# Performance work log

Measured on AMD Instinct MI355X. Metric: run time of the kernel, lower is better.

The kernel has to match this reference:

```python
import jax, jax.numpy as jnp
import numpy as np

B, L, D, V = 512, 128, 512, 100000

def setup_inputs() -> dict:
    key = jax.random.key(0)
    ks = jax.random.split(key, 8)
    return {
        "t1s": jax.random.randint(ks[0], (B,), 0, V),
        "t2s": jax.random.randint(ks[1], (B,), 0, V),
        "t1_contexts": jax.random.randint(ks[2], (B, L), 0, V),
        "t2_contexts": jax.random.randint(ks[3], (B, L), 0, V),
        "embed_table": jax.random.normal(ks[4], (V, D), dtype=jnp.float32),
        "att_mat": jax.random.normal(ks[5], (D, D), dtype=jnp.float32) * (6.0 / (D + D)) ** 0.5,
        "w_pred": jax.random.normal(ks[6], (D, 1), dtype=jnp.float32) * 0.02,
        "b_pred": jnp.zeros((1,), dtype=jnp.float32),
    }

def _frob_normalize(x):
    # torch.norm(mat, p=2) is the Frobenius norm of the whole (L, D) matrix
    n = jnp.sqrt(jnp.sum(x * x, axis=(1, 2), keepdims=True))
    return x / n

def reference(t1s, t2s, t1_contexts, t2_contexts, embed_table, att_mat, w_pred, b_pred):
    # dropout is identity in eval mode; t1s/t2s embeddings are unused in the
    # 'dynamic' branch (dead code in the original forward).
    A = _frob_normalize(embed_table[t1_contexts])  # (B, L, D)
    Bm = _frob_normalize(embed_table[t2_contexts])  # (B, L, D)
    # batched bilinear attention: tanh(A @ att_mat @ B^T)
    S = jnp.tanh(jnp.einsum('bld,de,bme->blm', A, att_mat, Bm))  # (B, L, L)
    rows = jax.nn.softmax(jnp.mean(S, axis=2), axis=1)  # (B, L)
    cols = jax.nn.softmax(jnp.mean(S, axis=1), axis=1)  # (B, L)
    newA = jnp.einsum('bld,bl->bd', A, rows)   # (B, D)
    newB = jnp.einsum('bld,bl->bd', Bm, cols)  # (B, D)
    logits = ((newA * newB) @ w_pred + b_pred).reshape(-1)  # (B,)
    return logits, S
```

## Files before the change

kernel.cpp:

```cpp
#include <hip/hip_runtime.h>
#include <hip/hip_bf16.h>
#include <stdint.h>

#define NB 512
#define NL 128
#define ND 512

typedef __bf16 bf16;
typedef __bf16 bf16x8 __attribute__((ext_vector_type(8)));
typedef float  f32x4  __attribute__((ext_vector_type(4)));

#define GLDS(src, dst) __builtin_amdgcn_global_load_lds( \
    (const __attribute__((address_space(1))) void*)(src), \
    (__attribute__((address_space(3))) void*)(dst), 16, 0, 0)

__global__ __launch_bounds__(256) void k_attT(const float* __restrict__ att,
                                              bf16* __restrict__ attT) {
    int i = blockIdx.x * 256 + threadIdx.x;
    int n = i >> 9, k = i & 511;
    attT[i] = (bf16)att[k * 512 + n];
}

__global__ __launch_bounds__(512) void k_mega(
        const int* __restrict__ ctx1, const int* __restrict__ ctx2,
        const float* __restrict__ table, const bf16* __restrict__ attT,
        bf16* __restrict__ Ab, bf16* __restrict__ Bb,
        float* __restrict__ Sout, const float* __restrict__ w_pred,
        const float* __restrict__ b_pred, float* __restrict__ logits) {
    const int b = blockIdx.x, row0 = b * NL, tid = threadIdx.x;
    const int lane = tid & 63, w = tid >> 6;
    const int lm = lane & 15, quad = lane >> 4;

    __shared__ __align__(16) char smem[163840];
    bf16* sA0 = (bf16*)smem;
    bf16* sA1 = (bf16*)(smem + 8192);
    bf16* sT0 = (bf16*)(smem + 16384);
    bf16* sT1 = (bf16*)(smem + 49152);
    bf16* Tls = (bf16*)smem;
    bf16* sB0 = (bf16*)(smem + 131072);
    bf16* sB1 = (bf16*)(smem + 139264);
    bf16* sC0 = (bf16*)(smem + 147456);
    bf16* sC1 = (bf16*)(smem + 155648);
    float* red  = (float*)(smem + 1024);
    float* rowb = (float*)smem;
    float* colb = (float*)(smem + 2048);
    float* wrow = (float*)(smem + 3072);
    float* wcol = (float*)(smem + 3584);
    float* red2 = (float*)(smem + 2048);

    const int r8 = tid >> 6, c8 = tid & 63;
    float pa = 0.f, pb = 0.f;
    #pragma unroll 4
    for (int j = 0; j < 16; ++j) {
        int l = j * 8 + r8;
        int ia = ctx1[row0 + l], ib = ctx2[row0 + l];
        const float4* ra = (const float4*)table + (size_t)ia * (ND / 4) + c8 * 2;
        const float4* rb = (const float4*)table + (size_t)ib * (ND / 4) + c8 * 2;
        float4 a0 = ra[0], a1 = ra[1];
        float4 b0 = rb[0], b1 = rb[1];
        pa += a0.x*a0.x + a0.y*a0.y + a0.z*a0.z + a0.w*a0.w
            + a1.x*a1.x + a1.y*a1.y + a1.z*a1.z + a1.w*a1.w;
        pb += b0.x*b0.x + b0.y*b0.y + b0.z*b0.z + b0.w*b0.w
            + b1.x*b1.x + b1.y*b1.y + b1.z*b1.z + b1.w*b1.w;
        union { bf16 h[8]; uint4 u; } ua, ub;
        ua.h[0]=(bf16)a0.x; ua.h[1]=(bf16)a0.y; ua.h[2]=(bf16)a0.z; ua.h[3]=(bf16)a0.w;
        ua.h[4]=(bf16)a1.x; ua.h[5]=(bf16)a1.y; ua.h[6]=(bf16)a1.z; ua.h[7]=(bf16)a1.w;
        ub.h[0]=(bf16)b0.x; ub.h[1]=(bf16)b0.y; ub.h[2]=(bf16)b0.z; ub.h[3]=(bf16)b0.w;
        ub.h[4]=(bf16)b1.x; ub.h[5]=(bf16)b1.y; ub.h[6]=(bf16)b1.z; ub.h[7]=(bf16)b1.w;
        *(uint4*)(Ab + (size_t)(row0 + l) * ND + c8 * 8) = ua.u;
        *(uint4*)(Bb + (size_t)(row0 + l) * ND + c8 * 8) = ub.u;
    }
    for (int o = 32; o; o >>= 1) { pa += __shfl_xor(pa, o); pb += __shfl_xor(pb, o); }
    if (lane == 0) { red[w * 2] = pa; red[w * 2 + 1] = pb; }
    __syncthreads();
    float ssA = 0.f, ssB = 0.f;
    #pragma unroll
    for (int i = 0; i < 8; ++i) { ssA += red[i * 2]; ssB += red[i * 2 + 1]; }
    __syncthreads();

    const int wm1 = (w & 1) * 64;
    const int wn1 = (w >> 1) * 128;
    f32x4 acc1[4][8] = {};
    const int rA = tid >> 2, cA = tid & 3;

    GLDS(Ab + (size_t)(row0 + rA) * ND + cA * 8, sA0 + tid * 8);
    #pragma unroll
    for (int i = 0; i < 4; ++i) {
        int s = i * 512 + tid, r = s >> 2, c = s & 3;
        GLDS(attT + (size_t)r * ND + c * 8, sT0 + s * 8);
    }
    __syncthreads();

    for (int t = 0; t < 16; ++t) {
        if (t < 15) {
            const int k0 = (t + 1) * 32;
            bf16* dA = (t & 1) ? sA0 : sA1;
            bf16* dT = (t & 1) ? sT0 : sT1;
            GLDS(Ab + (size_t)(row0 + rA) * ND + k0 + cA * 8, dA + tid * 8);
            #pragma unroll
            for (int i = 0; i < 4; ++i) {
                int s = i * 512 + tid, r = s >> 2, c = s & 3;
                GLDS(attT + (size_t)r * ND + k0 + c * 8, dT + s * 8);
            }
        } else {
            GLDS(Bb + (size_t)(row0 + rA) * ND + cA * 8, sB0 + tid * 8);
            GLDS(Ab + (size_t)(row0 + rA) * ND + cA * 8, sC0 + tid * 8);
        }
        const bf16* A_ = (t & 1) ? sA1 : sA0;
        const bf16* T_ = (t & 1) ? sT1 : sT0;
        bf16x8 af[4], bfm[8];
        #pragma unroll
        for (int t4 = 0; t4 < 4; ++t4)
            af[t4] = *(const bf16x8*)&A_[(wm1 + t4 * 16 + lm) * 32 + quad * 8];
        #pragma unroll
        for (int t8 = 0; t8 < 8; ++t8)
            bfm[t8] = *(const bf16x8*)&T_[(wn1 + t8 * 16 + lm) * 32 + quad * 8];
        #pragma unroll
        for (int im = 0; im < 4; ++im)
            #pragma unroll
            for (int jn = 0; jn < 8; ++jn)
                acc1[im][jn] = __builtin_amdgcn_mfma_f32_16x16x32_bf16(
                    af[im], bfm[jn], acc1[im][jn], 0, 0, 0);
        __syncthreads();
    }

    #pragma unroll
    for (int im = 0; im < 4; ++im)
    #pragma unroll
    for (int jn = 0; jn < 8; ++jn)
    #pragma unroll
    for (int p = 0; p < 4; ++p) {
        int m = wm1 + im * 16 + quad * 4 + p;
        int n = wn1 + jn * 16 + lm;
        int ks = n >> 5, kq = (n >> 3) & 3, e = n & 7;
        int pos = kq ^ ((m >> 2) & 3);
        Tls[ks * 4096 + m * 32 + pos * 8 + e] = (bf16)acc1[im][jn][p];
    }
    __syncthreads();

    const int wm2 = (w & 1) * 64;
    const int wn2 = (w >> 1) * 32;
    f32x4 acc2[4][2] = {}, accG[4][2] = {};

    for (int t = 0; t < 16; ++t) {
        if (t < 15) {
            bf16* dB = (t & 1) ? sB0 : sB1;
            bf16* dC = (t & 1) ? sC0 : sC1;
            GLDS(Bb + (size_t)(row0 + rA) * ND + (t + 1) * 32 + cA * 8, dB + tid * 8);
            GLDS(Ab + (size_t)(row0 + rA) * ND + (t + 1) * 32 + cA * 8, dC + tid * 8);
        }
        const bf16* B_ = (t & 1) ? sB1 : sB0;
        const bf16* C_ = (t & 1) ? sC1 : sC0;
        float4 w0 = *(const float4*)(w_pred + t * 32 + quad * 8);
        float4 w1 = *(const float4*)(w_pred + t * 32 + quad * 8 + 4);
        float wv[8] = {w0.x, w0.y, w0.z, w0.w, w1.x, w1.y, w1.z, w1.w};
        bf16x8 af[4], af2[4], bf2[2], bfw[2];
        #pragma unroll
        for (int t4 = 0; t4 < 4; ++t4) {
            int r = wm2 + t4 * 16 + lm;
            af[t4]  = *(const bf16x8*)&Tls[t * 4096 + r * 32 + ((quad ^ ((r >> 2) & 3))) * 8];
            af2[t4] = *(const bf16x8*)&C_[r * 32 + quad * 8];
        }
        #pragma unroll
        for (int t2 = 0; t2 < 2; ++t2) {
            bf2[t2] = *(const bf16x8*)&B_[(wn2 + t2 * 16 + lm) * 32 + quad * 8];
            #pragma unroll
            for (int j = 0; j < 8; ++j)
                bfw[t2][j] = (bf16)((float)bf2[t2][j] * wv[j]);
        }
        #pragma unroll
        for (int im = 0; im < 4; ++im)
            #pragma unroll
            for (int jn = 0; jn < 2; ++jn) {
                acc2[im][jn] = __builtin_amdgcn_mfma_f32_16x16x32_bf16(
                    af[im], bf2[jn], acc2[im][jn], 0, 0, 0);
                accG[im][jn] = __builtin_amdgcn_mfma_f32_16x16x32_bf16(
                    af2[im], bfw[jn], accG[im][jn], 0, 0, 0);
            }
        __syncthreads();
    }

    const float sc = rsqrtf(ssA * ssB);
    float* __restrict__ Sb = Sout + (size_t)b * NL * NL;
    #pragma unroll
    for (int im = 0; im < 4; ++im)
    #pragma unroll
    for (int jn = 0; jn < 2; ++jn)
    #pragma unroll
    for (int p = 0; p < 4; ++p) {
        float v = tanhf(acc2[im][jn][p] * sc);
        acc2[im][jn][p] = v;
        int m = wm2 + im * 16 + quad * 4 + p;
        int n = wn2 + jn * 16 + lm;
        __builtin_nontemporal_store(v, &Sb[m * NL + n]);
    }
    #pragma unroll
    for (int im = 0; im < 4; ++im)
    #pragma unroll
    for (int p = 0; p < 4; ++p) {
        float r = acc2[im][0][p] + acc2[im][1][p];
        r += __shfl_xor(r, 1); r += __shfl_xor(r, 2);
        r += __shfl_xor(r, 4); r += __shfl_xor(r, 8);
        if (lm == 0) rowb[(w >> 1) * NL + wm2 + im * 16 + quad * 4 + p] = r;
    }
    #pragma unroll
    for (int jn = 0; jn < 2; ++jn) {
        float cv = 0.f;
        #pragma unroll
        for (int im = 0; im < 4; ++im)
            #pragma unroll
            for (int p = 0; p < 4; ++p) cv += acc2[im][jn][p];
        cv += __shfl_xor(cv, 16); cv += __shfl_xor(cv, 32);
        if (quad == 0) colb[(w & 1) * NL + wn2 + jn * 16 + lm] = cv;
    }
    __syncthreads();

    if (tid < 64) {
        float a  = (rowb[tid] + rowb[NL + tid] + rowb[2 * NL + tid] + rowb[3 * NL + tid]) * (1.f / NL);
        float c2 = (rowb[tid + 64] + rowb[NL + tid + 64] + rowb[2 * NL + tid + 64] + rowb[3 * NL + tid + 64]) * (1.f / NL);
        float mx = fmaxf(a, c2);
        for (int o = 32; o; o >>= 1) mx = fmaxf(mx, __shfl_xor(mx, o));
        float e0 = expf(a - mx), e1 = expf(c2 - mx);
        float s = e0 + e1;
        for (int o = 32; o; o >>= 1) s += __shfl_xor(s, o);
        float inv = 1.f / s;
        wrow[tid] = e0 * inv; wrow[tid + 64] = e1 * inv;
    } else if (tid < 128) {
        int q = tid - 64;
        float a  = (colb[q] + colb[NL + q]) * (1.f / NL);
        float c2 = (colb[q + 64] + colb[NL + q + 64]) * (1.f / NL);
        float mx = fmaxf(a, c2);
        for (int o = 32; o; o >>= 1) mx = fmaxf(mx, __shfl_xor(mx, o));
        float e0 = expf(a - mx), e1 = expf(c2 - mx);
        float s = e0 + e1;
        for (int o = 32; o; o >>= 1) s += __shfl_xor(s, o);
        float inv = 1.f / s;
        wcol[q] = e0 * inv; wcol[q + 64] = e1 * inv;
    }
    __syncthreads();

    float wc0 = wcol[wn2 + lm], wc1 = wcol[wn2 + 16 + lm];
    float g = 0.f;
    #pragma unroll
    for (int im = 0; im < 4; ++im)
    #pragma unroll
    for (int p = 0; p < 4; ++p) {
        float wr = wrow[wm2 + im * 16 + quad * 4 + p];
        g += wr * (wc0 * accG[im][0][p] + wc1 * accG[im][1][p]);
    }
    for (int o = 32; o; o >>= 1) g += __shfl_xor(g, o);
    if (lane == 0) red2[w] = g;
    __syncthreads();
    if (tid == 0) {
        float tot = 0.f;
        #pragma unroll
        for (int i = 0; i < 8; ++i) tot += red2[i];
        logits[b] = tot * sc + b_pred[0];
    }
}

extern "C" void kernel_launch(void* const* d_in, const int* in_sizes, int n_in,
                              void* d_out, int out_size, void* d_ws, size_t ws_size,
                              hipStream_t stream) {
    const int*   t1c = (const int*)d_in[2];
    const int*   t2c = (const int*)d_in[3];
    const float* emb = (const float*)d_in[4];
    const float* att = (const float*)d_in[5];
    const float* wp  = (const float*)d_in[6];
    const float* bp  = (const float*)d_in[7];

    float* out    = (float*)d_out;
    float* logits = out;
    float* S      = out + NB;

    char* ws = (char*)d_ws;
    bf16*  Ab   = (bf16*)(ws);
    bf16*  Bb   = (bf16*)(ws + 67108864);
    bf16*  attT = (bf16*)(ws + 134217728);

    k_attT<<<dim3(1024), 256, 0, stream>>>(att, attT);
    k_mega<<<dim3(NB), 512, 0, stream>>>(t1c, t2c, emb, attT, Ab, Bb,
                                         S, wp, bp, logits);
}
```

Measured before the change: 387.8 us.

## Chunk the attention GEMM over N to cut shared memory and raise occupancy

The first GEMM (A @ att) is now computed in four 128-column chunks, and each chunk is immediately consumed by the second GEMM against B, so the full T matrix no longer has to sit in shared memory. This shrinks LDS from 160KB to about 68KB, uses XOR-swizzled 64-wide K tiles, and adds a launch-bounds occupancy hint. The logits path is rebuilt as explicit weighted sums of A and B rows read back from global memory, replacing the extra MFMA accumulation. The trade-offs are no double buffering (load then sync each step), more barriers, and an extra global reread of A and B.

```diff
diff --git a/kernel.cpp b/kernel.cpp
--- a/kernel.cpp
+++ b/kernel.cpp
@@ -21,7 +21,7 @@
     attT[i] = (bf16)att[k * 512 + n];
 }
 
-__global__ __launch_bounds__(512) void k_mega(
+__global__ __launch_bounds__(512, 4) void k_mega(
         const int* __restrict__ ctx1, const int* __restrict__ ctx2,
         const float* __restrict__ table, const bf16* __restrict__ attT,
         bf16* __restrict__ Ab, bf16* __restrict__ Bb,
@@ -30,23 +30,21 @@
     const int b = blockIdx.x, row0 = b * NL, tid = threadIdx.x;
     const int lane = tid & 63, w = tid >> 6;
     const int lm = lane & 15, quad = lane >> 4;
-
-    __shared__ __align__(16) char smem[163840];
-    bf16* sA0 = (bf16*)smem;
-    bf16* sA1 = (bf16*)(smem + 8192);
-    bf16* sT0 = (bf16*)(smem + 16384);
-    bf16* sT1 = (bf16*)(smem + 49152);
-    bf16* Tls = (bf16*)smem;
-    bf16* sB0 = (bf16*)(smem + 131072);
-    bf16* sB1 = (bf16*)(smem + 139264);
-    bf16* sC0 = (bf16*)(smem + 147456);
-    bf16* sC1 = (bf16*)(smem + 155648);
-    float* red  = (float*)(smem + 1024);
-    float* rowb = (float*)smem;
-    float* colb = (float*)(smem + 2048);
-    float* wrow = (float*)(smem + 3072);
-    float* wcol = (float*)(smem + 3584);
-    float* red2 = (float*)(smem + 2048);
+    const int wm = (w & 1) * 64;
+    const int wn = (w >> 1) * 32;
+
+    __shared__ __align__(16) char smem[69888];
+    bf16* st0 = (bf16*)smem;
+    bf16* st1 = (bf16*)(smem + 16384);
+    bf16* Tch = (bf16*)(smem + 32768);
+    float* pA   = (float*)smem;
+    float* pB   = (float*)(smem + 16384);
+    float* red  = (float*)(smem + 65536);
+    float* red2 = (float*)(smem + 65600);
+    float* rowb = (float*)(smem + 65664);
+    float* colb = (float*)(smem + 67712);
+    float* wrow = (float*)(smem + 68736);
+    float* wcol = (float*)(smem + 69248);
 
     const int r8 = tid >> 6, c8 = tid & 63;
     float pa = 0.f, pb = 0.f;
@@ -76,107 +74,84 @@
     float ssA = 0.f, ssB = 0.f;
     #pragma unroll
     for (int i = 0; i < 8; ++i) { ssA += red[i * 2]; ssB += red[i * 2 + 1]; }
-    __syncthreads();
-
-    const int wm1 = (w & 1) * 64;
-    const int wn1 = (w >> 1) * 128;
-    f32x4 acc1[4][8] = {};
-    const int rA = tid >> 2, cA = tid & 3;
-
-    GLDS(Ab + (size_t)(row0 + rA) * ND + cA * 8, sA0 + tid * 8);
-    #pragma unroll
-    for (int i = 0; i < 4; ++i) {
-        int s = i * 512 + tid, r = s >> 2, c = s & 3;
-        GLDS(attT + (size_t)r * ND + c * 8, sT0 + s * 8);
-    }
-    __syncthreads();
-
-    for (int t = 0; t < 16; ++t) {
-        if (t < 15) {
-            const int k0 = (t + 1) * 32;
-            bf16* dA = (t & 1) ? sA0 : sA1;
-            bf16* dT = (t & 1) ? sT0 : sT1;
-            GLDS(Ab + (size_t)(row0 + rA) * ND + k0 + cA * 8, dA + tid * 8);
-            #pragma unroll
-            for (int i = 0; i < 4; ++i) {
-                int s = i * 512 + tid, r = s >> 2, c = s & 3;
-                GLDS(attT + (size_t)r * ND + k0 + c * 8, dT + s * 8);
-            }
-        } else {
-            GLDS(Bb + (size_t)(row0 + rA) * ND + cA * 8, sB0 + tid * 8);
-            GLDS(Ab + (size_t)(row0 + rA) * ND + cA * 8, sC0 + tid * 8);
-        }
-        const bf16* A_ = (t & 1) ? sA1 : sA0;
-        const bf16* T_ = (t & 1) ? sT1 : sT0;
-        bf16x8 af[4], bfm[8];
-        #pragma unroll
-        for (int t4 = 0; t4 < 4; ++t4)
-            af[t4] = *(const bf16x8*)&A_[(wm1 + t4 * 16 + lm) * 32 + quad * 8];
-        #pragma unroll
-        for (int t8 = 0; t8 < 8; ++t8)
-            bfm[t8] = *(const bf16x8*)&T_[(wn1 + t8 * 16 + lm) * 32 + quad * 8];
+
+    f32x4 accS[4][2] = {};
+
+    for (int nc = 0; nc < 4; ++nc) {
+        const bf16* attN = attT + (size_t)(nc * 128) * ND;
+        f32x4 acc1[4][2] = {};
+
+        for (int t8 = 0; t8 < 8; ++t8) {
+            const int k0 = t8 * 64;
+            #pragma unroll
+            for (int i = 0; i < 2; ++i) {
+                int s = i * 512 + tid, r = s >> 3, c = (s & 7) ^ (r & 7);
+                GLDS(Ab + (size_t)(row0 + r) * ND + k0 + c * 8, st0 + s * 8);
+                GLDS(attN + (size_t)r * ND + k0 + c * 8, st1 + s * 8);
+            }
+            __syncthreads();
+            #pragma unroll
+            for (int kk = 0; kk < 2; ++kk) {
+                bf16x8 af[4], bf2[2];
+                const int ca = (kk * 4 + quad) ^ (lm & 7);
+                #pragma unroll
+                for (int t4 = 0; t4 < 4; ++t4)
+                    af[t4] = *(const bf16x8*)&st0[(wm + t4 * 16 + lm) * 64 + ca * 8];
+                #pragma unroll
+                for (int t2 = 0; t2 < 2; ++t2)
+                    bf2[t2] = *(const bf16x8*)&st1[(wn + t2 * 16 + lm) * 64 + ca * 8];
+                #pragma unroll
+                for (int im = 0; im < 4; ++im)
+                    #pragma unroll
+                    for (int jn = 0; jn < 2; ++jn)
+                        acc1[im][jn] = __builtin_amdgcn_mfma_f32_16x16x32_bf16(
+                            af[im], bf2[jn], acc1[im][jn], 0, 0, 0);
+            }
+            __syncthreads();
+        }
+
+        #pragma unroll
+        for (int i = 0; i < 2; ++i) {
+            int s = i * 512 + tid, r = s >> 3, c = (s & 7) ^ (r & 7);
+            GLDS(Bb + (size_t)(row0 + r) * ND + nc * 128 + c * 8, st0 + s * 8);
+            GLDS(Bb + (size_t)(row0 + r) * ND + nc * 128 + 64 + c * 8, st1 + s * 8);
+        }
         #pragma unroll
         for (int im = 0; im < 4; ++im)
-            #pragma unroll
-            for (int jn = 0; jn < 8; ++jn)
-                acc1[im][jn] = __builtin_amdgcn_mfma_f32_16x16x32_bf16(
-                    af[im], bfm[jn], acc1[im][jn], 0, 0, 0);
+        #pragma unroll
+        for (int jn = 0; jn < 2; ++jn)
+        #pragma unroll
+        for (int p = 0; p < 4; ++p) {
+            int m = wm + im * 16 + quad * 4 + p;
+            int n = wn + jn * 16 + lm;
+            int ks = n >> 6, c = n & 63;
+            int pos = (((c >> 3) ^ (m & 7)) << 3) + (c & 7);
+            Tch[ks * 8192 + m * 64 + pos] = (bf16)acc1[im][jn][p];
+        }
         __syncthreads();
-    }
-
-    #pragma unroll
-    for (int im = 0; im < 4; ++im)
-    #pragma unroll
-    for (int jn = 0; jn < 8; ++jn)
-    #pragma unroll
-    for (int p = 0; p < 4; ++p) {
-        int m = wm1 + im * 16 + quad * 4 + p;
-        int n = wn1 + jn * 16 + lm;
-        int ks = n >> 5, kq = (n >> 3) & 3, e = n & 7;
-        int pos = kq ^ ((m >> 2) & 3);
-        Tls[ks * 4096 + m * 32 + pos * 8 + e] = (bf16)acc1[im][jn][p];
-    }
-    __syncthreads();
-
-    const int wm2 = (w & 1) * 64;
-    const int wn2 = (w >> 1) * 32;
-    f32x4 acc2[4][2] = {}, accG[4][2] = {};
-
-    for (int t = 0; t < 16; ++t) {
-        if (t < 15) {
-            bf16* dB = (t & 1) ? sB0 : sB1;
-            bf16* dC = (t & 1) ? sC0 : sC1;
-            GLDS(Bb + (size_t)(row0 + rA) * ND + (t + 1) * 32 + cA * 8, dB + tid * 8);
-            GLDS(Ab + (size_t)(row0 + rA) * ND + (t + 1) * 32 + cA * 8, dC + tid * 8);
-        }
-        const bf16* B_ = (t & 1) ? sB1 : sB0;
-        const bf16* C_ = (t & 1) ? sC1 : sC0;
-        float4 w0 = *(const float4*)(w_pred + t * 32 + quad * 8);
-        float4 w1 = *(const float4*)(w_pred + t * 32 + quad * 8 + 4);
-        float wv[8] = {w0.x, w0.y, w0.z, w0.w, w1.x, w1.y, w1.z, w1.w};
-        bf16x8 af[4], af2[4], bf2[2], bfw[2];
-        #pragma unroll
-        for (int t4 = 0; t4 < 4; ++t4) {
-            int r = wm2 + t4 * 16 + lm;
-            af[t4]  = *(const bf16x8*)&Tls[t * 4096 + r * 32 + ((quad ^ ((r >> 2) & 3))) * 8];
-            af2[t4] = *(const bf16x8*)&C_[r * 32 + quad * 8];
-        }
-        #pragma unroll
-        for (int t2 = 0; t2 < 2; ++t2) {
-            bf2[t2] = *(const bf16x8*)&B_[(wn2 + t2 * 16 + lm) * 32 + quad * 8];
-            #pragma unroll
-            for (int j = 0; j < 8; ++j)
-                bfw[t2][j] = (bf16)((float)bf2[t2][j] * wv[j]);
-        }
-        #pragma unroll
-        for (int im = 0; im < 4; ++im)
-            #pragma unroll
-            for (int jn = 0; jn < 2; ++jn) {
-                acc2[im][jn] = __builtin_amdgcn_mfma_f32_16x16x32_bf16(
-                    af[im], bf2[jn], acc2[im][jn], 0, 0, 0);
-                accG[im][jn] = __builtin_amdgcn_mfma_f32_16x16x32_bf16(
-                    af2[im], bfw[jn], accG[im][jn], 0, 0, 0);
-            }
+
+        #pragma unroll
+        for (int th = 0; th < 2; ++th) {
+            const bf16* Bs_ = th ? st1 : st0;
+            const bf16* Tk  = Tch + th * 8192;
+            #pragma unroll
+            for (int kk = 0; kk < 2; ++kk) {
+                bf16x8 af[4], bf2[2];
+                const int ca = (kk * 4 + quad) ^ (lm & 7);
+                #pragma unroll
+                for (int t4 = 0; t4 < 4; ++t4)
+                    af[t4] = *(const bf16x8*)&Tk[(wm + t4 * 16 + lm) * 64 + ca * 8];
+                #pragma unroll
+                for (int t2 = 0; t2 < 2; ++t2)
+                    bf2[t2] = *(const bf16x8*)&Bs_[(wn + t2 * 16 + lm) * 64 + ca * 8];
+                #pragma unroll
+                for (int im = 0; im < 4; ++im)
+                    #pragma unroll
+                    for (int jn = 0; jn < 2; ++jn)
+                        accS[im][jn] = __builtin_amdgcn_mfma_f32_16x16x32_bf16(
+                            af[im], bf2[jn], accS[im][jn], 0, 0, 0);
+            }
+        }
         __syncthreads();
     }
 
@@ -188,20 +163,20 @@
     for (int jn = 0; jn < 2; ++jn)
     #pragma unroll
     for (int p = 0; p < 4; ++p) {
-        float v = tanhf(acc2[im][jn][p] * sc);
-        acc2[im][jn][p] = v;
-        int m = wm2 + im * 16 + quad * 4 + p;
-        int n = wn2 + jn * 16 + lm;
+        float v = tanhf(accS[im][jn][p] * sc);
+        accS[im][jn][p] = v;
+        int m = wm + im * 16 + quad * 4 + p;
+        int n = wn + jn * 16 + lm;
         __builtin_nontemporal_store(v, &Sb[m * NL + n]);
     }
     #pragma unroll
     for (int im = 0; im < 4; ++im)
     #pragma unroll
     for (int p = 0; p < 4; ++p) {
-        float r = acc2[im][0][p] + acc2[im][1][p];
+        float r = accS[im][0][p] + accS[im][1][p];
         r += __shfl_xor(r, 1); r += __shfl_xor(r, 2);
         r += __shfl_xor(r, 4); r += __shfl_xor(r, 8);
-        if (lm == 0) rowb[(w >> 1) * NL + wm2 + im * 16 + quad * 4 + p] = r;
+        if (lm == 0) rowb[(w >> 1) * NL + wm + im * 16 + quad * 4 + p] = r;
     }
     #pragma unroll
     for (int jn = 0; jn < 2; ++jn) {
@@ -209,9 +184,9 @@
         #pragma unroll
         for (int im = 0; im < 4; ++im)
             #pragma unroll
-            for (int p = 0; p < 4; ++p) cv += acc2[im][jn][p];
+            for (int p = 0; p < 4; ++p) cv += accS[im][jn][p];
         cv += __shfl_xor(cv, 16); cv += __shfl_xor(cv, 32);
-        if (quad == 0) colb[(w & 1) * NL + wn2 + jn * 16 + lm] = cv;
+        if (quad == 0) colb[(w & 1) * NL + wn + jn * 16 + lm] = cv;
     }
     __syncthreads();
 
@@ -239,23 +214,43 @@
     }
     __syncthreads();
 
-    float wc0 = wcol[wn2 + lm], wc1 = wcol[wn2 + 16 + lm];
-    float g = 0.f;
-    #pragma unroll
-    for (int im = 0; im < 4; ++im)
-    #pragma unroll
-    for (int p = 0; p < 4; ++p) {
-        float wr = wrow[wm2 + im * 16 + quad * 4 + p];
-        g += wr * (wc0 * accG[im][0][p] + wc1 * accG[im][1][p]);
-    }
-    for (int o = 32; o; o >>= 1) g += __shfl_xor(g, o);
-    if (lane == 0) red2[w] = g;
-    __syncthreads();
-    if (tid == 0) {
-        float tot = 0.f;
-        #pragma unroll
-        for (int i = 0; i < 8; ++i) tot += red2[i];
-        logits[b] = tot * sc + b_pred[0];
+    const int c = tid & 63, g = tid >> 6;
+    const bf16* __restrict__ Abase = Ab + (size_t)b * NL * ND;
+    const bf16* __restrict__ Bbase = Bb + (size_t)b * NL * ND;
+    float aacc[8] = {}, bacc[8] = {};
+    for (int l = g; l < NL; l += 8) {
+        float wr = wrow[l], wc = wcol[l];
+        bf16x8 va = *(const bf16x8*)(Abase + (size_t)l * ND + c * 8);
+        bf16x8 vb = *(const bf16x8*)(Bbase + (size_t)l * ND + c * 8);
+        #pragma unroll
+        for (int j = 0; j < 8; ++j) {
+            aacc[j] += wr * (float)va[j];
+            bacc[j] += wc * (float)vb[j];
+        }
+    }
+    #pragma unroll
+    for (int j = 0; j < 8; ++j) {
+        pA[g * ND + c * 8 + j] = aacc[j];
+        pB[g * ND + c * 8 + j] = bacc[j];
+    }
+    __syncthreads();
+
+    if (tid < 64) {
+        float dot = 0.f;
+        #pragma unroll
+        for (int j = 0; j < 8; ++j) {
+            int d = tid * 8 + j;
+            float na = 0.f, nb = 0.f;
+            #pragma unroll
+            for (int g2 = 0; g2 < 8; ++g2) {
+                na += pA[g2 * ND + d];
+                nb += pB[g2 * ND + d];
+            }
+            dot += na * nb * w_pred[d];
+        }
+        for (int o = 32; o; o >>= 1) dot += __shfl_xor(dot, o);
+        if (tid == 0)
+            logits[b] = dot * rsqrtf(ssA) * rsqrtf(ssB) + b_pred[0];
     }
 }
 
```

New measurement: 453.9 us. 17.1% more time.

## Swizzle LDS tiles, use fine-grained vmcnt waits and raw barriers with setprio

Applied to the files above, without the earlier changes.

The K-loop tiles for A, attT, B and C are now stored in LDS with an XOR swizzle on the 16-byte chunk index, so the MFMA fragment reads avoid bank conflicts. The full __syncthreads after each prefetch is replaced by explicit s_waitcnt vmcnt counts plus s_barrier, so the next stage's global->LDS loads can stay in flight while the current stage is consumed. MFMA sections are also bracketed with s_setprio. The reduction scratch is moved so it no longer overlaps the staging buffers. The hand-picked vmcnt counts depend on exactly how the compiler emits the loads, so a wrong count could read stale LDS.

```diff
diff --git a/kernel.cpp b/kernel.cpp
--- a/kernel.cpp
+++ b/kernel.cpp
@@ -30,23 +30,26 @@
     const int b = blockIdx.x, row0 = b * NL, tid = threadIdx.x;
     const int lane = tid & 63, w = tid >> 6;
     const int lm = lane & 15, quad = lane >> 4;
+    const int wm  = (w & 1) * 64;
+    const int wn1 = (w >> 1) * 128;
+    const int wn2 = (w >> 1) * 32;
 
     __shared__ __align__(16) char smem[163840];
-    bf16* sA0 = (bf16*)smem;
-    bf16* sA1 = (bf16*)(smem + 8192);
-    bf16* sT0 = (bf16*)(smem + 16384);
-    bf16* sT1 = (bf16*)(smem + 49152);
-    bf16* Tls = (bf16*)smem;
-    bf16* sB0 = (bf16*)(smem + 131072);
-    bf16* sB1 = (bf16*)(smem + 139264);
-    bf16* sC0 = (bf16*)(smem + 147456);
-    bf16* sC1 = (bf16*)(smem + 155648);
-    float* red  = (float*)(smem + 1024);
+    bf16* stA0 = (bf16*)smem;
+    bf16* stA1 = (bf16*)(smem + 8192);
+    bf16* stT0 = (bf16*)(smem + 16384);
+    bf16* stT1 = (bf16*)(smem + 49152);
+    float* red = (float*)(smem + 81920);
+    bf16* Tls  = (bf16*)smem;
+    bf16* sB0  = (bf16*)(smem + 131072);
+    bf16* sB1  = (bf16*)(smem + 139264);
+    bf16* sC0  = (bf16*)(smem + 147456);
+    bf16* sC1  = (bf16*)(smem + 155648);
     float* rowb = (float*)smem;
     float* colb = (float*)(smem + 2048);
     float* wrow = (float*)(smem + 3072);
     float* wcol = (float*)(smem + 3584);
-    float* red2 = (float*)(smem + 2048);
+    float* red2 = (float*)(smem + 4096);
 
     const int r8 = tid >> 6, c8 = tid & 63;
     float pa = 0.f, pb = 0.f;
@@ -76,52 +79,56 @@
     float ssA = 0.f, ssB = 0.f;
     #pragma unroll
     for (int i = 0; i < 8; ++i) { ssA += red[i * 2]; ssB += red[i * 2 + 1]; }
-    __syncthreads();
-
-    const int wm1 = (w & 1) * 64;
-    const int wn1 = (w >> 1) * 128;
+
+    #define STAGE1(k0, dA, dT) do {                                          \
+        { int r_ = tid >> 2, sl_ = tid & 3, cs_ = sl_ ^ ((r_ >> 1) & 3);     \
+          GLDS(Ab + (size_t)(row0 + r_) * ND + (k0) + cs_ * 8, (dA) + tid * 8); } \
+        _Pragma("unroll")                                                    \
+        for (int i_ = 0; i_ < 4; ++i_) {                                     \
+            int s_ = i_ * 512 + tid, r_ = s_ >> 2, sl_ = s_ & 3;             \
+            int cs_ = sl_ ^ ((r_ >> 1) & 3);                                 \
+            GLDS(attT + (size_t)r_ * ND + (k0) + cs_ * 8, (dT) + s_ * 8); }  \
+    } while (0)
+    #define STAGE2(k0, dB, dC) do {                                          \
+        int r_ = tid >> 2, sl_ = tid & 3, cs_ = sl_ ^ ((r_ >> 1) & 3);       \
+        GLDS(Bb + (size_t)(row0 + r_) * ND + (k0) + cs_ * 8, (dB) + tid * 8);\
+        GLDS(Ab + (size_t)(row0 + r_) * ND + (k0) + cs_ * 8, (dC) + tid * 8);\
+    } while (0)
+
     f32x4 acc1[4][8] = {};
-    const int rA = tid >> 2, cA = tid & 3;
-
-    GLDS(Ab + (size_t)(row0 + rA) * ND + cA * 8, sA0 + tid * 8);
-    #pragma unroll
-    for (int i = 0; i < 4; ++i) {
-        int s = i * 512 + tid, r = s >> 2, c = s & 3;
-        GLDS(attT + (size_t)r * ND + c * 8, sT0 + s * 8);
-    }
-    __syncthreads();
+    STAGE1(0, stA0, stT0);
 
     for (int t = 0; t < 16; ++t) {
         if (t < 15) {
-            const int k0 = (t + 1) * 32;
-            bf16* dA = (t & 1) ? sA0 : sA1;
-            bf16* dT = (t & 1) ? sT0 : sT1;
-            GLDS(Ab + (size_t)(row0 + rA) * ND + k0 + cA * 8, dA + tid * 8);
-            #pragma unroll
-            for (int i = 0; i < 4; ++i) {
-                int s = i * 512 + tid, r = s >> 2, c = s & 3;
-                GLDS(attT + (size_t)r * ND + k0 + c * 8, dT + s * 8);
-            }
+            STAGE1((t + 1) * 32, (t & 1) ? stA0 : stA1, (t & 1) ? stT0 : stT1);
+            asm volatile("s_waitcnt vmcnt(5)" ::: "memory");
         } else {
-            GLDS(Bb + (size_t)(row0 + rA) * ND + cA * 8, sB0 + tid * 8);
-            GLDS(Ab + (size_t)(row0 + rA) * ND + cA * 8, sC0 + tid * 8);
-        }
-        const bf16* A_ = (t & 1) ? sA1 : sA0;
-        const bf16* T_ = (t & 1) ? sT1 : sT0;
+            STAGE2(0, sB0, sC0);
+            asm volatile("s_waitcnt vmcnt(2)" ::: "memory");
+        }
+        __builtin_amdgcn_s_barrier();
+        const bf16* A_ = (t & 1) ? stA1 : stA0;
+        const bf16* T_ = (t & 1) ? stT1 : stT0;
         bf16x8 af[4], bfm[8];
         #pragma unroll
-        for (int t4 = 0; t4 < 4; ++t4)
-            af[t4] = *(const bf16x8*)&A_[(wm1 + t4 * 16 + lm) * 32 + quad * 8];
-        #pragma unroll
-        for (int t8 = 0; t8 < 8; ++t8)
-            bfm[t8] = *(const bf16x8*)&T_[(wn1 + t8 * 16 + lm) * 32 + quad * 8];
+        for (int t4 = 0; t4 < 4; ++t4) {
+            int R = wm + t4 * 16 + lm;
+            af[t4] = *(const bf16x8*)&A_[R * 32 + (quad ^ ((R >> 1) & 3)) * 8];
+        }
+        #pragma unroll
+        for (int t8 = 0; t8 < 8; ++t8) {
+            int R = wn1 + t8 * 16 + lm;
+            bfm[t8] = *(const bf16x8*)&T_[R * 32 + (quad ^ ((R >> 1) & 3)) * 8];
+        }
+        __builtin_amdgcn_s_setprio(1);
         #pragma unroll
         for (int im = 0; im < 4; ++im)
             #pragma unroll
             for (int jn = 0; jn < 8; ++jn)
                 acc1[im][jn] = __builtin_amdgcn_mfma_f32_16x16x32_bf16(
                     af[im], bfm[jn], acc1[im][jn], 0, 0, 0);
-        __syncthreads();
+        __builtin_amdgcn_s_setprio(0);
+        __builtin_amdgcn_s_barrier();
     }
 
     #pragma unroll
@@ -130,7 +137,7 @@
     for (int jn = 0; jn < 8; ++jn)
     #pragma unroll
     for (int p = 0; p < 4; ++p) {
-        int m = wm1 + im * 16 + quad * 4 + p;
+        int m = wm + im * 16 + quad * 4 + p;
         int n = wn1 + jn * 16 + lm;
         int ks = n >> 5, kq = (n >> 3) & 3, e = n & 7;
         int pos = kq ^ ((m >> 2) & 3);
@@ -138,17 +145,16 @@
     }
     __syncthreads();
 
-    const int wm2 = (w & 1) * 64;
-    const int wn2 = (w >> 1) * 32;
     f32x4 acc2[4][2] = {}, accG[4][2] = {};
 
     for (int t = 0; t < 16; ++t) {
         if (t < 15) {
-            bf16* dB = (t & 1) ? sB0 : sB1;
-            bf16* dC = (t & 1) ? sC0 : sC1;
-            GLDS(Bb + (size_t)(row0 + rA) * ND + (t + 1) * 32 + cA * 8, dB + tid * 8);
-            GLDS(Ab + (size_t)(row0 + rA) * ND + (t + 1) * 32 + cA * 8, dC + tid * 8);
-        }
+            STAGE2((t + 1) * 32, (t & 1) ? sB0 : sB1, (t & 1) ? sC0 : sC1);
+            asm volatile("s_waitcnt vmcnt(2)" ::: "memory");
+        } else {
+            asm volatile("s_waitcnt vmcnt(0)" ::: "memory");
+        }
+        __builtin_amdgcn_s_barrier();
         const bf16* B_ = (t & 1) ? sB1 : sB0;
         const bf16* C_ = (t & 1) ? sC1 : sC0;
         float4 w0 = *(const float4*)(w_pred + t * 32 + quad * 8);
@@ -157,17 +163,19 @@
         bf16x8 af[4], af2[4], bf2[2], bfw[2];
         #pragma unroll
         for (int t4 = 0; t4 < 4; ++t4) {
-            int r = wm2 + t4 * 16 + lm;
-            af[t4]  = *(const bf16x8*)&Tls[t * 4096 + r * 32 + ((quad ^ ((r >> 2) & 3))) * 8];
-            af2[t4] = *(const bf16x8*)&C_[r * 32 + quad * 8];
+            int R = wm + t4 * 16 + lm;
+            af[t4]  = *(const bf16x8*)&Tls[t * 4096 + R * 32 + (quad ^ ((R >> 2) & 3)) * 8];
+            af2[t4] = *(const bf16x8*)&C_[R * 32 + (quad ^ ((R >> 1) & 3)) * 8];
         }
         #pragma unroll
         for (int t2 = 0; t2 < 2; ++t2) {
-            bf2[t2] = *(const bf16x8*)&B_[(wn2 + t2 * 16 + lm) * 32 + quad * 8];
+            int R = wn2 + t2 * 16 + lm;
+            bf2[t2] = *(const bf16x8*)&B_[R * 32 + (quad ^ ((R >> 1) & 3)) * 8];
             #pragma unroll
             for (int j = 0; j < 8; ++j)
                 bfw[t2][j] = (bf16)((float)bf2[t2][j] * wv[j]);
         }
+        __builtin_amdgcn_s_setprio(1);
         #pragma unroll
         for (int im = 0; im < 4; ++im)
             #pragma unroll
@@ -177,7 +185,8 @@
                 accG[im][jn] = __builtin_amdgcn_mfma_f32_16x16x32_bf16(
                     af2[im], bfw[jn], accG[im][jn], 0, 0, 0);
             }
-        __syncthreads();
+        __builtin_amdgcn_s_setprio(0);
+        __builtin_amdgcn_s_barrier();
     }
 
     const float sc = rsqrtf(ssA * ssB);
@@ -190,7 +199,7 @@
     for (int p = 0; p < 4; ++p) {
         float v = tanhf(acc2[im][jn][p] * sc);
         acc2[im][jn][p] = v;
-        int m = wm2 + im * 16 + quad * 4 + p;
+        int m = wm + im * 16 + quad * 4 + p;
         int n = wn2 + jn * 16 + lm;
         __builtin_nontemporal_store(v, &Sb[m * NL + n]);
     }
@@ -201,7 +210,7 @@
         float r = acc2[im][0][p] + acc2[im][1][p];
         r += __shfl_xor(r, 1); r += __shfl_xor(r, 2);
         r += __shfl_xor(r, 4); r += __shfl_xor(r, 8);
-        if (lm == 0) rowb[(w >> 1) * NL + wm2 + im * 16 + quad * 4 + p] = r;
+        if (lm == 0) rowb[(w >> 1) * NL + wm + im * 16 + quad * 4 + p] = r;
     }
     #pragma unroll
     for (int jn = 0; jn < 2; ++jn) {
@@ -245,7 +254,7 @@
     for (int im = 0; im < 4; ++im)
     #pragma unroll
     for (int p = 0; p < 4; ++p) {
-        float wr = wrow[wm2 + im * 16 + quad * 4 + p];
+        float wr = wrow[wm + im * 16 + quad * 4 + p];
         g += wr * (wc0 * accG[im][0][p] + wc1 * accG[im][1][p]);
     }
     for (int o = 32; o; o >>= 1) g += __shfl_xor(g, o);
```

New measurement: 388.2 us. About the same (+0.1%).
